# Optimization experiments

Hardware: AMD Instinct MI355X
Metric: run time of the kernel (lower is better)

## Reference

```python
import jax, jax.numpy as jnp
import numpy as np

GROUPS = 8   # GroupNorm groups used by create_pat_conv*_blocks(..., groups=8)
EPS = 1e-5
K = 20       # num_neighbor


def group_norm(x, gamma, beta):
    # x: [B, C, ...spatial]
    B, C = x.shape[0], x.shape[1]
    shape = x.shape
    xg = x.reshape(B, GROUPS, C // GROUPS, -1)
    m = xg.mean(axis=(2, 3), keepdims=True)
    v = ((xg - m) ** 2).mean(axis=(2, 3), keepdims=True)
    xg = (xg - m) * jax.lax.rsqrt(v + EPS)
    x = xg.reshape(shape)
    bshape = (1, C) + (1,) * (len(shape) - 2)
    return x * gamma.reshape(bshape) + beta.reshape(bshape)


def conv_block(x, w, b, gamma, beta):
    # pointwise (kernel-size 1) conv + GroupNorm + ELU, works for 1d and 2d spatial
    y = jnp.einsum('oc,bc...->bo...', w, x) + b.reshape((1, -1) + (1,) * (x.ndim - 2))
    return jax.nn.elu(group_norm(y, gamma, beta))


def knn_graph(points, k):
    # points: [B, 3, N] -> neighbor coords [B, 3, N, k] (self included, dilation=1)
    sq = jnp.sum(points * points, axis=1)                      # [B, N]
    inner = jnp.einsum('bci,bcj->bij', points, points)         # [B, N, N]
    dist = sq[:, :, None] + sq[:, None, :] - 2.0 * inner       # squared pairwise dist
    _, idx = jax.lax.top_k(-dist, k)                           # [B, N, k] smallest dists
    neighbors = jnp.take_along_axis(points[:, :, None, :], idx[:, None, :, :], axis=3)
    return neighbors                                           # [B, 3, N, k]


def setup_inputs() -> dict:
    key = jax.random.key(0)
    B, N = 4, 8192
    dims1 = [6, 32, 64]
    dims2 = [64, 512, 1024]
    keys = iter(jax.random.split(key, 32))
    inp = {"points": jax.random.normal(next(keys), (B, 3, N), dtype=jnp.float32)}
    for tag, dims in (("p1", dims1), ("p2", dims2)):
        for i in range(len(dims) - 1):
            cin, cout = dims[i], dims[i + 1]
            inp[f"{tag}_w{i}"] = jax.random.normal(next(keys), (cout, cin), dtype=jnp.float32) / np.float32(np.sqrt(cin))
            inp[f"{tag}_b{i}"] = jnp.zeros((cout,), dtype=jnp.float32)
            inp[f"{tag}_g{i}"] = jnp.ones((cout,), dtype=jnp.float32)
            inp[f"{tag}_beta{i}"] = jnp.zeros((cout,), dtype=jnp.float32)
    return inp


def reference(points, p1_w0, p1_b0, p1_g0, p1_beta0, p1_w1, p1_b1, p1_g1, p1_beta1,
              p2_w0, p2_b0, p2_g0, p2_beta0, p2_w1, p2_b1, p2_g1, p2_beta1):
    neighbors = knn_graph(points, K)                             # [B, 3, N, K]
    center = jnp.broadcast_to(points[:, :, :, None], neighbors.shape)
    x = jnp.concatenate([center, neighbors - center], axis=1)   # [B, 6, N, K]
    x = conv_block(x, p1_w0, p1_b0, p1_g0, p1_beta0)            # [B, 32, N, K]
    x = conv_block(x, p1_w1, p1_b1, p1_g1, p1_beta1)            # [B, 64, N, K]
    x = jnp.max(x, axis=2)                                      # [B, 64, K] (faithful to source: max over dim=2)
    x = conv_block(x, p2_w0, p2_b0, p2_g0, p2_beta0)            # [B, 512, K]
    x = conv_block(x, p2_w1, p2_b1, p2_g1, p2_beta1)            # [B, 1024, K]
    return x
```

## Files before the change

### kernel.cpp

```cpp
#include <hip/hip_runtime.h>
#include <math.h>

#define NPTS   8192
#define BATCH  4
#define KNN    20
#define NKTOT  (NPTS*KNN)
#define EPS    1e-5f
#define QCAP   56

typedef float v2f __attribute__((ext_vector_type(2)));

__device__ __forceinline__ float elu(float x) { return x > 0.0f ? x : expm1f(x); }
__device__ __forceinline__ float eluf(float x) { return x > 0.0f ? x : __expf(x) - 1.0f; }
__device__ __forceinline__ v2f splat2(float x) { v2f v; v.x = x; v.y = x; return v; }
__device__ __forceinline__ float rfl(float x) {
    return __uint_as_float(__builtin_amdgcn_readfirstlane(__float_as_uint(x)));
}

__device__ __forceinline__ unsigned fenc(float f) {
    unsigned b = __float_as_uint(f);
    return b ^ ((unsigned)(((int)b) >> 31) | 0x80000000u);
}
__device__ __forceinline__ float fdec(unsigned u) {
    unsigned b = (u & 0x80000000u) ? (u ^ 0x80000000u) : ~u;
    return __uint_as_float(b);
}

__global__ __launch_bounds__(256) void prep_kernel(const float* __restrict__ points,
                                                   float4* __restrict__ pts4)
{
    const int t = blockIdx.x * 256 + threadIdx.x;
    const int b = t >> 13, n = t & (NPTS - 1);
    const float* px = points + b * 3 * NPTS;
    float x = px[n], y = px[NPTS + n], z = px[2 * NPTS + n];
    pts4[t] = make_float4(x, y, z, -0.5f * (x * x + y * y + z * z));
}

__global__ __launch_bounds__(512, 8) void knn_kernel(const float4* __restrict__ pts4,
                                                     int* __restrict__ idx_out)
{
    __shared__ unsigned long long queue[32][QCAP];
    __shared__ int qcnt[32];
    __shared__ float gsh[2][32];

    const int tid  = threadIdx.x;
    const int lane = tid & 63;
    const int wv   = tid >> 6;
    const int oct  = wv >> 1;
    const int par  = wv & 1;
    const int b    = blockIdx.x >> 8;
    const int q0   = (blockIdx.x & 255) * 32 + oct * 8;
    const float4* pb = pts4 + b * NPTS;
    const int cbase = par * (NPTS / 2);

    if (tid < 32) qcnt[tid] = 0;

    float qx[8], qy[8], qz[8];
    v2f smax2[8];
#pragma unroll
    for (int q = 0; q < 8; ++q) {
        float4 qp = pb[q0 + q];
        qx[q] = rfl(qp.x); qy[q] = rfl(qp.y); qz[q] = rfl(qp.z);
        smax2[q] = splat2(-INFINITY);
    }

#pragma unroll 4
    for (int t = 0; t < NPTS / 2 / 128; ++t) {
        float4 p0 = pb[cbase + t * 128 + 2 * lane];
        float4 p1 = pb[cbase + t * 128 + 2 * lane + 1];
        v2f px = { p0.x, p1.x }, py = { p0.y, p1.y };
        v2f pz = { p0.z, p1.z }, pw = { p0.w, p1.w };
#pragma unroll
        for (int q = 0; q < 8; ++q) {
            v2f sv = __builtin_elementwise_fma(splat2(qx[q]), px,
                     __builtin_elementwise_fma(splat2(qy[q]), py,
                     __builtin_elementwise_fma(splat2(qz[q]), pz, pw)));
            smax2[q] = __builtin_elementwise_max(smax2[q], sv);
        }
    }

    float gloc[8];
#pragma unroll
    for (int q = 0; q < 8; ++q) {
        float v = fmaxf(smax2[q].x, smax2[q].y);
#pragma unroll
        for (int k = 2; k <= 64; k <<= 1)
#pragma unroll
            for (int j = k >> 1; j >= 1; j >>= 1) {
                float o = __shfl_xor(v, j);
                bool up = ((lane & k) == 0);
                bool keepmin = (((lane & j) == 0) == up);
                v = keepmin ? fminf(v, o) : fmaxf(v, o);
            }
        gloc[q] = __shfl(v, 44);
    }
    if (lane == 0) {
#pragma unroll
        for (int q = 0; q < 8; ++q) gsh[par][oct * 8 + q] = gloc[q];
    }
    __syncthreads();
    float sgate[8];
#pragma unroll
    for (int q = 0; q < 8; ++q) {
        float m = fmaxf(gsh[0][oct * 8 + q], gsh[1][oct * 8 + q]);
        sgate[q] = m - 1e-4f - 1e-5f * fabsf(m);
    }

    for (int t = 0; t < NPTS / 2 / 128; ++t) {
        float4 p0 = pb[cbase + t * 128 + 2 * lane];
        float4 p1 = pb[cbase + t * 128 + 2 * lane + 1];
        v2f px = { p0.x, p1.x }, py = { p0.y, p1.y };
        v2f pz = { p0.z, p1.z }, pw = { p0.w, p1.w };
        const int jb = cbase + t * 128 + 2 * lane;
#pragma unroll
        for (int q = 0; q < 8; ++q) {
            v2f sv = __builtin_elementwise_fma(splat2(qx[q]), px,
                     __builtin_elementwise_fma(splat2(qy[q]), py,
                     __builtin_elementwise_fma(splat2(qz[q]), pz, pw)));
            if (fmaxf(sv.x, sv.y) >= sgate[q]) {
#pragma unroll
                for (int h = 0; h < 2; ++h) {
                    float svh = h ? sv.y : sv.x;
                    if (svh >= sgate[q]) {
                        int slot = atomicAdd(&qcnt[oct * 8 + q], 1);
                        if (slot < QCAP) {
                            unsigned long long key =
                                ((unsigned long long)fenc(svh) << 32)
                                | (unsigned)(NPTS - 1 - (jb + h));
                            queue[oct * 8 + q][slot] = key;
                        }
                    }
                }
            }
        }
    }
    __syncthreads();

#pragma unroll
    for (int qq = 0; qq < 4; ++qq) {
        const int q = par * 4 + qq;
        int cq = qcnt[oct * 8 + q]; cq = cq < QCAP ? cq : QCAP;
        unsigned long long key = (lane < cq) ? queue[oct * 8 + q][lane] : 0ull;
#pragma unroll
        for (int k = 2; k <= 64; k <<= 1)
#pragma unroll
            for (int j = k >> 1; j >= 1; j >>= 1) {
                unsigned long long o = __shfl_xor(key, j);
                bool up = ((lane & k) == 0);
                bool keepmax = (((lane & j) == 0) == up);
                bool omax = o > key;
                key = (keepmax == omax) ? o : key;
            }
        if (lane < KNN)
            idx_out[(b * KNN + lane) * NPTS + (q0 + q)] =
                NPTS - 1 - (int)(unsigned)(key & 0xFFFFFFFFu);
    }
}

__global__ __launch_bounds__(256) void moments_x_kernel(const float* __restrict__ points,
                                                        const int* __restrict__ idx,
                                                        float* __restrict__ sums1p)
{
    const int t = blockIdx.x * 256 + threadIdx.x;
    const int b = blockIdx.x / 640;
    const int r = t - b * NKTOT;
    const int n = r & (NPTS - 1);
    const float* px = points + b * 3 * NPTS;
    const int j = idx[t];
    float cx = px[n], cy = px[NPTS + n], cz = px[2 * NPTS + n];
    float v[27];
    v[0] = cx; v[1] = cy; v[2] = cz;
    v[3] = px[j] - cx; v[4] = px[NPTS + j] - cy; v[5] = px[2 * NPTS + j] - cz;
    int p = 6;
#pragma unroll
    for (int d = 0; d < 6; ++d)
#pragma unroll
        for (int e = d; e < 6; ++e) v[p++] = v[d] * v[e];
#pragma unroll
    for (int i = 0; i < 27; ++i)
        for (int o = 32; o > 0; o >>= 1) v[i] += __shfl_xor(v[i], o);

    __shared__ float red[4][27];
    const int lane = threadIdx.x & 63, w = threadIdx.x >> 6;
    if (lane == 0)
#pragma unroll
        for (int i = 0; i < 27; ++i) red[w][i] = v[i];
    __syncthreads();
    if (threadIdx.x < 27) {
        float acc = red[0][threadIdx.x] + red[1][threadIdx.x] + red[2][threadIdx.x] + red[3][threadIdx.x];
        int slot = blockIdx.x & 63;
        atomicAdd(&sums1p[(slot * BATCH + b) * 27 + threadIdx.x], acc);
    }
}

__global__ void finalize1_kernel(const float* __restrict__ sums1p,
                                 const float* __restrict__ w1, const float* __restrict__ b1,
                                 const float* __restrict__ g1, const float* __restrict__ beta1,
                                 float* __restrict__ w1f)
{
    __shared__ float S[BATCH][27];
    const int t = threadIdx.x;
    if (t < 108) {
        int b = t / 27, i = t % 27;
        float acc = 0.f;
        for (int s = 0; s < 64; ++s) acc += sums1p[(s * BATCH + b) * 27 + i];
        S[b][i] = acc;
    }
    __syncthreads();
    const int b = t >> 5, c = t & 31;
    const float invS = 1.0f / (float)NKTOT;
    float Ex[6], M[6][6];
#pragma unroll
    for (int d = 0; d < 6; ++d) Ex[d] = S[b][d] * invS;
    int p = 6;
#pragma unroll
    for (int d = 0; d < 6; ++d)
#pragma unroll
        for (int e = d; e < 6; ++e) { float v = S[b][p++] * invS; M[d][e] = v; M[e][d] = v; }
    const int g = c >> 2;
    float msum = 0.f, qsum = 0.f;
    for (int cc = g * 4; cc < g * 4 + 4; ++cc) {
        float w[6];
#pragma unroll
        for (int d = 0; d < 6; ++d) w[d] = w1[cc * 6 + d];
        float dotEx = 0.f;
#pragma unroll
        for (int d = 0; d < 6; ++d) dotEx += w[d] * Ex[d];
        float Ey = dotEx + b1[cc];
        float Ey2 = 0.f;
#pragma unroll
        for (int d = 0; d < 6; ++d)
#pragma unroll
            for (int e = 0; e < 6; ++e) Ey2 += w[d] * w[e] * M[d][e];
        Ey2 += 2.0f * b1[cc] * dotEx + b1[cc] * b1[cc];
        msum += Ey; qsum += Ey2;
    }
    float m = msum * 0.25f;
    float var = qsum * 0.25f - m * m;
    float inv = rsqrtf(var + EPS);
    float s = g1[c] * inv;
    float tt = s * (b1[c] - m) + beta1[c];
    float* o = w1f + (b * 32 + c) * 8;
#pragma unroll
    for (int d = 0; d < 6; ++d) o[d] = s * w1[c * 6 + d];
    o[6] = tt; o[7] = 0.f;
}

__global__ __launch_bounds__(256, 5) void fused_main_kernel(
    const float4* __restrict__ pts4, const int* __restrict__ idxb,
    const float* __restrict__ w1f, const float* __restrict__ w2, const float* __restrict__ b2,
    float* __restrict__ sums2p, unsigned int* __restrict__ maxenc, unsigned int* __restrict__ minenc)
{
    __shared__ __align__(16) float w2t[32 * 64];
    __shared__ __align__(16) float z1s[32 * 128];
    __shared__ __align__(16) float4 w1s4[64];
    __shared__ float b2s[64];
    __shared__ float redmx[256], redmn[256], sqred[128];

    const int t   = threadIdx.x;
    const int blk = blockIdx.x;
    const int nc  = blk & 15;
    const int k   = (blk >> 4) % 20;
    const int b   = blk / 320;

    for (int i = t; i < 512; i += 256) {
        float4 v = ((const float4*)w2)[i];
        int c = i >> 3, kq = (i & 7) * 4;
        w2t[(kq + 0) * 64 + c] = v.x; w2t[(kq + 1) * 64 + c] = v.y;
        w2t[(kq + 2) * 64 + c] = v.z; w2t[(kq + 3) * 64 + c] = v.w;
    }
    if (t < 64) { w1s4[t] = ((const float4*)w1f)[b * 64 + t]; b2s[t] = b2[t]; }

    const int wvi  = t >> 6;
    const int nf   = t & 127;
    const int cgf  = t >> 7;
    const int cq   = t & 15;
    const int ng   = t >> 4;
    const int c0   = cq * 4;
    const int n0   = ng * 8;
    const float4* pb = pts4 + b * NPTS;
    const int nbase = nc * 512;
    const int* idxrow = idxb + (b * KNN + k) * NPTS;

    float mx[4], mn[4];
#pragma unroll
    for (int ci = 0; ci < 4; ++ci) { mx[ci] = -INFINITY; mn[ci] = INFINITY; }
    float gs = 0.f, gq = 0.f;

    for (int ph = 0; ph < 4; ++ph) {
        const int n = nbase + ph * 128 + nf;
        const int j = idxrow[n];
        float4 c4 = pb[n];
        float4 e4 = pb[j];
        float x0[6] = { c4.x, c4.y, c4.z, e4.x - c4.x, e4.y - c4.y, e4.z - c4.z };

        __syncthreads();
#pragma unroll
        for (int jj = 0; jj < 16; ++jj) {
            int c = cgf * 16 + jj;
            float4 wA = w1s4[c * 2 + 0];
            float4 wB = w1s4[c * 2 + 1];
            float z = wB.z;
            z = fmaf(wA.x, x0[0], z); z = fmaf(wA.y, x0[1], z); z = fmaf(wA.z, x0[2], z);
            z = fmaf(wA.w, x0[3], z); z = fmaf(wB.x, x0[4], z); z = fmaf(wB.y, x0[5], z);
            z1s[c * 128 + nf] = eluf(z);
        }
        __syncthreads();

        float acc[4][8];
#pragma unroll
        for (int ci = 0; ci < 4; ++ci) {
            float bb = b2s[c0 + ci];
#pragma unroll
            for (int pj = 0; pj < 8; ++pj) acc[ci][pj] = bb;
        }
#pragma unroll
        for (int kk = 0; kk < 32; ++kk) {
            float4 av = *(const float4*)&w2t[kk * 64 + c0];
            float4 z0 = *(const float4*)&z1s[kk * 128 + n0];
            float4 z1v = *(const float4*)&z1s[kk * 128 + n0 + 4];
            float avv[4] = { av.x, av.y, av.z, av.w };
            float zvv[8] = { z0.x, z0.y, z0.z, z0.w, z1v.x, z1v.y, z1v.z, z1v.w };
#pragma unroll
            for (int ci = 0; ci < 4; ++ci)
#pragma unroll
                for (int pj = 0; pj < 8; ++pj) acc[ci][pj] = fmaf(avv[ci], zvv[pj], acc[ci][pj]);
        }
#pragma unroll
        for (int ci = 0; ci < 4; ++ci)
#pragma unroll
            for (int pj = 0; pj < 8; ++pj) {
                float v = acc[ci][pj];
                gs += v; gq = fmaf(v, v, gq);
                mx[ci] = fmaxf(mx[ci], v); mn[ci] = fminf(mn[ci], v);
            }
    }

#pragma unroll
    for (int m = 16; m <= 32; m <<= 1) {
#pragma unroll
        for (int ci = 0; ci < 4; ++ci) {
            mx[ci] = fmaxf(mx[ci], __shfl_xor(mx[ci], m));
            mn[ci] = fminf(mn[ci], __shfl_xor(mn[ci], m));
        }
        gs += __shfl_xor(gs, m);
        gq += __shfl_xor(gq, m);
    }
    if ((t & 63) < 16) {
#pragma unroll
        for (int ci = 0; ci < 4; ++ci) {
            redmx[wvi * 64 + cq * 4 + ci] = mx[ci];
            redmn[wvi * 64 + cq * 4 + ci] = mn[ci];
        }
        sqred[(wvi * 16 + cq) * 2 + 0] = gs;
        sqred[(wvi * 16 + cq) * 2 + 1] = gq;
    }
    __syncthreads();
    if (t < 64) {
        float m = fmaxf(fmaxf(redmx[t], redmx[64 + t]), fmaxf(redmx[128 + t], redmx[192 + t]));
        atomicMax(&maxenc[(b * 64 + t) * KNN + k], fenc(m));
    } else if (t < 128) {
        int c = t - 64;
        float m = fminf(fminf(redmn[c], redmn[64 + c]), fminf(redmn[128 + c], redmn[192 + c]));
        atomicMin(&minenc[(b * 64 + c) * KNN + k], fenc(m));
    } else if (t < 144) {
        int i2 = t - 128, g = i2 >> 1, w = i2 & 1;
        float v = 0.f;
#pragma unroll
        for (int wv2 = 0; wv2 < 4; ++wv2)
            v += sqred[(wv2 * 16 + 2 * g) * 2 + w] + sqred[(wv2 * 16 + 2 * g + 1) * 2 + w];
        int slot = blk & 63;
        atomicAdd(&sums2p[((slot * BATCH + b) * 8 + g) * 2 + w], v);
    }
}

__global__ void build_m1_kernel(const float* __restrict__ sums2p,
                                const unsigned int* __restrict__ maxenc,
                                const unsigned int* __restrict__ minenc,
                                const float* __restrict__ gamma, const float* __restrict__ beta,
                                float* __restrict__ m1)
{
    const int t = blockIdx.x * 256 + threadIdx.x;
    const int b = t / 1280;
    const int r = t - b * 1280;
    const int c = r / 20;
    const int g = c >> 3;
    float s = 0.f, q = 0.f;
    for (int sl = 0; sl < 64; ++sl) {
        s += sums2p[((sl * BATCH + b) * 8 + g) * 2 + 0];
        q += sums2p[((sl * BATCH + b) * 8 + g) * 2 + 1];
    }
    const float cnt = 8.0f * (float)NKTOT;
    float m = s / cnt;
    float var = q / cnt - m * m;
    float inv = rsqrtf(var + EPS);
    float sc = gamma[c] * inv;
    float tt = beta[c] - sc * m;
    float y = (sc >= 0.f) ? fdec(maxenc[t]) : fdec(minenc[t]);
    m1[t] = elu(sc * y + tt);
}

template <int CIN, int SLOTS>
__global__ void p2_gemm_kernel(const float* __restrict__ zin, const float* __restrict__ w,
                               const float* __restrict__ bias, float* __restrict__ yout,
                               float* __restrict__ sumsp, int chans_per_group)
{
    const int t = blockIdx.x * 256 + threadIdx.x;
    const int per_b = (gridDim.x * 256) / BATCH;
    const int b = t / per_b;
    const int r = t - b * per_b;
    const int o = r / 20;
    const int k = r - o * 20;
    const float* zb = zin + b * CIN * 20;
    const float* wrow = w + o * CIN;
    float acc = bias[o];
    for (int c = 0; c < CIN; c += 4) {
        float4 wv = *(const float4*)&wrow[c];
        acc += wv.x * zb[(c + 0) * 20 + k] + wv.y * zb[(c + 1) * 20 + k]
             + wv.z * zb[(c + 2) * 20 + k] + wv.w * zb[(c + 3) * 20 + k];
    }
    yout[t] = acc;

    __shared__ float ls[16];
    if (threadIdx.x < 16) ls[threadIdx.x] = 0.f;
    __syncthreads();
    const int g = o / chans_per_group;
    atomicAdd(&ls[g * 2 + 0], acc);
    atomicAdd(&ls[g * 2 + 1], acc * acc);
    __syncthreads();
    if (threadIdx.x < 16) {
        int slot = blockIdx.x & (SLOTS - 1);
        atomicAdd(&sumsp[(slot * BATCH + b) * 16 + threadIdx.x], ls[threadIdx.x]);
    }
}

template <int SLOTS>
__global__ void p2_finalize_kernel(const float* __restrict__ y, const float* __restrict__ sumsp,
                                   const float* __restrict__ gamma, const float* __restrict__ beta,
                                   float* __restrict__ z, int chans_per_group, float cnt)
{
    const int t = blockIdx.x * 256 + threadIdx.x;
    const int per_b = (gridDim.x * 256) / BATCH;
    const int b = t / per_b;
    const int r = t - b * per_b;
    const int o = r / 20;
    const int g = o / chans_per_group;
    float s = 0.f, q = 0.f;
    for (int sl = 0; sl < SLOTS; ++sl) {
        s += sumsp[(sl * BATCH + b) * 16 + g * 2 + 0];
        q += sumsp[(sl * BATCH + b) * 16 + g * 2 + 1];
    }
    float m = s / cnt;
    float var = q / cnt - m * m;
    float inv = rsqrtf(var + EPS);
    float v = gamma[o] * inv * (y[t] - m) + beta[o];
    z[t] = elu(v);
}

extern "C" void kernel_launch(void* const* d_in, const int* in_sizes, int n_in,
                              void* d_out, int out_size, void* d_ws, size_t ws_size,
                              hipStream_t stream)
{
    const float* points  = (const float*)d_in[0];
    const float* p1_w0   = (const float*)d_in[1];
    const float* p1_b0   = (const float*)d_in[2];
    const float* p1_g0   = (const float*)d_in[3];
    const float* p1_bt0  = (const float*)d_in[4];
    const float* p1_w1   = (const float*)d_in[5];
    const float* p1_b1   = (const float*)d_in[6];
    const float* p1_g1   = (const float*)d_in[7];
    const float* p1_bt1  = (const float*)d_in[8];
    const float* p2_w0   = (const float*)d_in[9];
    const float* p2_b0   = (const float*)d_in[10];
    const float* p2_g0   = (const float*)d_in[11];
    const float* p2_bt0  = (const float*)d_in[12];
    const float* p2_w1   = (const float*)d_in[13];
    const float* p2_b1   = (const float*)d_in[14];
    const float* p2_g1   = (const float*)d_in[15];
    const float* p2_bt1  = (const float*)d_in[16];
    float* out = (float*)d_out;

    float* ws = (float*)d_ws;
    int*      idx     = (int*)ws;
    float*    sums1p  = ws + 655360;
    float*    sums2p  = sums1p + 6912;
    float*    sumsAp  = sums2p + 4096;
    float*    sumsBp  = sumsAp + 1024;
    unsigned* maxenc  = (unsigned*)(sumsBp + 1024);
    unsigned* minenc  = maxenc + 5120;
    float*    w1f     = (float*)(minenc + 5120);
    float*    m1      = w1f + 1024;
    float*    yp2a    = m1 + 5120;
    float*    zp2a    = yp2a + 40960;
    float*    yp2b    = zp2a + 40960;
    float4*   pts4    = (float4*)yp2a;

    hipMemsetAsync(sums1p, 0, (6912 + 4096 + 1024 + 1024 + 5120) * sizeof(float), stream);
    hipMemsetAsync(minenc, 0xFF, 5120 * sizeof(unsigned), stream);

    prep_kernel<<<128, 256, 0, stream>>>(points, pts4);
    knn_kernel<<<1024, 512, 0, stream>>>(pts4, idx);
    moments_x_kernel<<<2560, 256, 0, stream>>>(points, idx, sums1p);
    finalize1_kernel<<<1, 128, 0, stream>>>(sums1p, p1_w0, p1_b0, p1_g0, p1_bt0, w1f);
    fused_main_kernel<<<1280, 256, 0, stream>>>(pts4, idx, w1f, p1_w1, p1_b1,
                                                sums2p, maxenc, minenc);
    build_m1_kernel<<<20, 256, 0, stream>>>(sums2p, maxenc, minenc, p1_g1, p1_bt1, m1);
    p2_gemm_kernel<64, 16><<<160, 256, 0, stream>>>(m1, p2_w0, p2_b0, yp2a, sumsAp, 64);
    p2_finalize_kernel<16><<<160, 256, 0, stream>>>(yp2a, sumsAp, p2_g0, p2_bt0, zp2a, 64, 1280.0f);
    p2_gemm_kernel<512, 16><<<320, 256, 0, stream>>>(zp2a, p2_w1, p2_b1, yp2b, sumsBp, 128);
    p2_finalize_kernel<16><<<320, 256, 0, stream>>>(yp2b, sumsBp, p2_g1, p2_bt1, out, 128, 2560.0f);
}
```

Before: 287.8 us.

## Shrink KNN blocks to 256 threads, per-wave queues; batch moments per thread

The KNN kernel now runs 256-thread blocks covering 16 queries, with each wave pair merging per-lane maxima through shared memory to compute the gate. Each wave also gets its own candidate queue (capacity 28), and the two queues are merged before the bitonic sort. This is meant to cut LDS atomic contention and block size so more blocks can be resident. The moments kernel now has each thread accumulate 8 elements, reading from the packed float4 points. That reduces the number of blocks, shuffle reductions and global atomics. The risk is a per-wave queue overflow at 28 entries, which would silently drop candidates.

```diff
diff --git a/kernel.cpp b/kernel.cpp
--- a/kernel.cpp
+++ b/kernel.cpp
@@ -6,7 +6,7 @@
 #define KNN    20
 #define NKTOT  (NPTS*KNN)
 #define EPS    1e-5f
-#define QCAP   56
+#define QC     28
 
 typedef float v2f __attribute__((ext_vector_type(2)));
 
@@ -36,20 +36,21 @@
     pts4[t] = make_float4(x, y, z, -0.5f * (x * x + y * y + z * z));
 }
 
-__global__ __launch_bounds__(512, 8) void knn_kernel(const float4* __restrict__ pts4,
+__global__ __launch_bounds__(256, 8) void knn_kernel(const float4* __restrict__ pts4,
                                                      int* __restrict__ idx_out)
 {
-    __shared__ unsigned long long queue[32][QCAP];
+    __shared__ unsigned long long queue[32][QC];
+    __shared__ float smaxs[4][8][64];
+    __shared__ float gates[2][8];
     __shared__ int qcnt[32];
-    __shared__ float gsh[2][32];
 
     const int tid  = threadIdx.x;
     const int lane = tid & 63;
     const int wv   = tid >> 6;
     const int oct  = wv >> 1;
     const int par  = wv & 1;
-    const int b    = blockIdx.x >> 8;
-    const int q0   = (blockIdx.x & 255) * 32 + oct * 8;
+    const int b    = blockIdx.x >> 9;
+    const int q0   = (blockIdx.x & 511) * 16 + oct * 8;
     const float4* pb = pts4 + b * NPTS;
     const int cbase = par * (NPTS / 2);
 
@@ -78,11 +79,14 @@
             smax2[q] = __builtin_elementwise_max(smax2[q], sv);
         }
     }
-
-    float gloc[8];
-#pragma unroll
-    for (int q = 0; q < 8; ++q) {
-        float v = fmaxf(smax2[q].x, smax2[q].y);
+#pragma unroll
+    for (int q = 0; q < 8; ++q) smaxs[wv][q][lane] = fmaxf(smax2[q].x, smax2[q].y);
+    __syncthreads();
+
+#pragma unroll
+    for (int qq = 0; qq < 4; ++qq) {
+        const int q = par * 4 + qq;
+        float v = fmaxf(smaxs[2 * oct][q][lane], smaxs[2 * oct + 1][q][lane]);
 #pragma unroll
         for (int k = 2; k <= 64; k <<= 1)
 #pragma unroll
@@ -92,19 +96,13 @@
                 bool keepmin = (((lane & j) == 0) == up);
                 v = keepmin ? fminf(v, o) : fmaxf(v, o);
             }
-        gloc[q] = __shfl(v, 44);
-    }
-    if (lane == 0) {
-#pragma unroll
-        for (int q = 0; q < 8; ++q) gsh[par][oct * 8 + q] = gloc[q];
+        float m = __shfl(v, 44);
+        if (lane == 0) gates[oct][q] = m - 1e-4f - 1e-5f * fabsf(m);
     }
     __syncthreads();
     float sgate[8];
 #pragma unroll
-    for (int q = 0; q < 8; ++q) {
-        float m = fmaxf(gsh[0][oct * 8 + q], gsh[1][oct * 8 + q]);
-        sgate[q] = m - 1e-4f - 1e-5f * fabsf(m);
-    }
+    for (int q = 0; q < 8; ++q) sgate[q] = gates[oct][q];
 
     for (int t = 0; t < NPTS / 2 / 128; ++t) {
         float4 p0 = pb[cbase + t * 128 + 2 * lane];
@@ -122,12 +120,12 @@
                 for (int h = 0; h < 2; ++h) {
                     float svh = h ? sv.y : sv.x;
                     if (svh >= sgate[q]) {
-                        int slot = atomicAdd(&qcnt[oct * 8 + q], 1);
-                        if (slot < QCAP) {
+                        int slot = atomicAdd(&qcnt[wv * 8 + q], 1);
+                        if (slot < QC) {
                             unsigned long long key =
                                 ((unsigned long long)fenc(svh) << 32)
                                 | (unsigned)(NPTS - 1 - (jb + h));
-                            queue[oct * 8 + q][slot] = key;
+                            queue[wv * 8 + q][slot] = key;
                         }
                     }
                 }
@@ -139,8 +137,11 @@
 #pragma unroll
     for (int qq = 0; qq < 4; ++qq) {
         const int q = par * 4 + qq;
-        int cq = qcnt[oct * 8 + q]; cq = cq < QCAP ? cq : QCAP;
-        unsigned long long key = (lane < cq) ? queue[oct * 8 + q][lane] : 0ull;
+        int cA = qcnt[(2 * oct) * 8 + q];     cA = cA < QC ? cA : QC;
+        int cB = qcnt[(2 * oct + 1) * 8 + q]; cB = cB < QC ? cB : QC;
+        unsigned long long key = 0ull;
+        if (lane < cA)           key = queue[(2 * oct) * 8 + q][lane];
+        else if (lane < cA + cB) key = queue[(2 * oct + 1) * 8 + q][lane - cA];
 #pragma unroll
         for (int k = 2; k <= 64; k <<= 1)
 #pragma unroll
@@ -157,25 +158,34 @@
     }
 }
 
-__global__ __launch_bounds__(256) void moments_x_kernel(const float* __restrict__ points,
+__global__ __launch_bounds__(256) void moments_x_kernel(const float4* __restrict__ pts4,
                                                         const int* __restrict__ idx,
                                                         float* __restrict__ sums1p)
 {
-    const int t = blockIdx.x * 256 + threadIdx.x;
-    const int b = blockIdx.x / 640;
-    const int r = t - b * NKTOT;
-    const int n = r & (NPTS - 1);
-    const float* px = points + b * 3 * NPTS;
-    const int j = idx[t];
-    float cx = px[n], cy = px[NPTS + n], cz = px[2 * NPTS + n];
+    const int b  = blockIdx.x / 80;
+    const int r0 = (blockIdx.x - b * 80) * 2048;
+    const float4* pb = pts4 + b * NPTS;
+    const int* ib = idx + b * NKTOT;
+
     float v[27];
-    v[0] = cx; v[1] = cy; v[2] = cz;
-    v[3] = px[j] - cx; v[4] = px[NPTS + j] - cy; v[5] = px[2 * NPTS + j] - cz;
-    int p = 6;
-#pragma unroll
-    for (int d = 0; d < 6; ++d)
-#pragma unroll
-        for (int e = d; e < 6; ++e) v[p++] = v[d] * v[e];
+#pragma unroll
+    for (int i = 0; i < 27; ++i) v[i] = 0.f;
+
+    for (int e = 0; e < 8; ++e) {
+        const int id = r0 + e * 256 + threadIdx.x;
+        const int n = id & (NPTS - 1);
+        const int j = ib[id];
+        float4 c4 = pb[n];
+        float4 e4 = pb[j];
+        float x[6] = { c4.x, c4.y, c4.z, e4.x - c4.x, e4.y - c4.y, e4.z - c4.z };
+        int p = 6;
+#pragma unroll
+        for (int d = 0; d < 6; ++d) {
+            v[d] += x[d];
+#pragma unroll
+            for (int ee = d; ee < 6; ++ee) v[p++] += x[d] * x[ee];
+        }
+    }
 #pragma unroll
     for (int i = 0; i < 27; ++i)
         for (int o = 32; o > 0; o >>= 1) v[i] += __shfl_xor(v[i], o);
@@ -499,8 +509,8 @@
     hipMemsetAsync(minenc, 0xFF, 5120 * sizeof(unsigned), stream);
 
     prep_kernel<<<128, 256, 0, stream>>>(points, pts4);
-    knn_kernel<<<1024, 512, 0, stream>>>(pts4, idx);
-    moments_x_kernel<<<2560, 256, 0, stream>>>(points, idx, sums1p);
+    knn_kernel<<<2048, 256, 0, stream>>>(pts4, idx);
+    moments_x_kernel<<<320, 256, 0, stream>>>(pts4, idx, sums1p);
     finalize1_kernel<<<1, 128, 0, stream>>>(sums1p, p1_w0, p1_b0, p1_g0, p1_bt0, w1f);
     fused_main_kernel<<<1280, 256, 0, stream>>>(pts4, idx, w1f, p1_w1, p1_b1,
                                                 sums2p, maxenc, minenc);
```

New measurement: 264.3 us. 8.2% less time.
